# Optimization experiments

Measured on AMD Instinct MI355X. Metric: run time of the kernel, lower is better.

## Reference

```python
import jax, jax.numpy as jnp
import numpy as np

N = 4096        # nodes == batch_size (GFN operates on dense N x N adjacency)
E = 65536       # edges per view (avg degree 16)
IN = 512        # per-view input feature dim
HV = [128, 64]  # per-view GCN dims
HM = [64, 64]   # fused-graph GCN dims
VIEWS = 3


def setup_inputs() -> dict:
    key = jax.random.key(0)
    ks = iter(jax.random.split(key, 64))

    def xavier(shape):
        lim = float(np.sqrt(6.0 / (shape[0] + shape[1])))
        return jax.random.uniform(next(ks), shape, minval=-lim, maxval=lim, dtype=jnp.float32)

    inp = {}
    for v in range(VIEWS):
        inp[f"x{v}"] = jax.random.normal(next(ks), (N, IN), dtype=jnp.float32)
        inp[f"src{v}"] = jax.random.randint(next(ks), (E,), 0, N, dtype=jnp.int32)
        inp[f"dst{v}"] = jax.random.randint(next(ks), (E,), 0, N, dtype=jnp.int32)
        inp[f"Wv{v}0"] = xavier((IN, HV[0]))
        inp[f"bv{v}0"] = jnp.zeros((HV[0],), jnp.float32)
        inp[f"Wv{v}1"] = xavier((HV[0], HV[1]))
        inp[f"bv{v}1"] = jnp.zeros((HV[1],), jnp.float32)
        inp[f"Wf{v}"] = xavier((HV[1], HV[1]))  # FeatureFusion weight
    # GFN: Linear(N -> N/2) -> ReLU -> Linear(N/2 -> N)
    inp["Wg1"] = xavier((N, N // 2)); inp["bg1"] = jnp.zeros((N // 2,), jnp.float32)
    inp["Wg2"] = xavier((N // 2, N)); inp["bg2"] = jnp.zeros((N,), jnp.float32)
    # fused-graph GCN layers
    inp["Wm0"] = xavier((HV[1], HM[0])); inp["bm0"] = jnp.zeros((HM[0],), jnp.float32)
    inp["Wm1"] = xavier((HM[0], HM[1])); inp["bm1"] = jnp.zeros((HM[1],), jnp.float32)
    return inp


def _deg_norms(src, dst):
    # DGL GraphConv norm='both': scale by out-deg(src)^-1/2 and in-deg(dst)^-1/2, degrees clamped to >=1
    ones = jnp.ones(src.shape[0], jnp.float32)
    dout = jnp.maximum(jax.ops.segment_sum(ones, src, num_segments=N), 1.0)
    din = jnp.maximum(jax.ops.segment_sum(ones, dst, num_segments=N), 1.0)
    return dout ** -0.5, din ** -0.5


def _gconv(x, W, b, src, dst, do_isqrt, di_isqrt, act):
    h = (x * do_isqrt[:, None]) @ W            # [N, out] (W commutes with row scaling)
    agg = jax.ops.segment_sum(h[src], dst, num_segments=N)
    h = agg * di_isqrt[:, None] + b
    return act(h)


def reference(x0, x1, x2, src0, dst0, src1, dst1, src2, dst2,
              Wv00, bv00, Wv01, bv01, Wv10, bv10, Wv11, bv11, Wv20, bv20, Wv21, bv21,
              Wf0, Wf1, Wf2, Wg1, bg1, Wg2, bg2, Wm0, bm0, Wm1, bm1):
    ident = lambda t: t
    xs = [x0, x1, x2]
    edges = [(src0, dst0), (src1, dst1), (src2, dst2)]
    Wv = [(Wv00, bv00, Wv01, bv01), (Wv10, bv10, Wv11, bv11), (Wv20, bv20, Wv21, bv21)]
    Wf = [Wf0, Wf1, Wf2]

    # per-view GCN stacks (relu on first layer, identity on last)
    feats = []
    for v in range(VIEWS):
        src, dst = edges[v]
        do_i, di_i = _deg_norms(src, dst)
        W0, b0, W1, b1 = Wv[v]
        f = _gconv(xs[v], W0, b0, src, dst, do_i, di_i, jax.nn.relu)
        f = _gconv(f, W1, b1, src, dst, do_i, di_i, ident)
        feats.append(f)

    # FeatureFusion (dropout omitted for determinism): sum(f @ Wf), softmax over features, relu
    z = feats[0] @ Wf[0] + feats[1] @ Wf[1] + feats[2] @ Wf[2]
    z = jax.nn.relu(jax.nn.softmax(z, axis=1))

    # consensus graph: sum of per-view dense adjacencies -> GFN -> clamp -> round(+0.1)
    adj = jnp.zeros((N, N), jnp.float32)
    for src, dst in edges:
        adj = adj + jnp.zeros((N, N), jnp.float32).at[src, dst].set(1.0)
    fused = jax.nn.relu(adj @ Wg1 + bg1) @ Wg2 + bg2
    fused = jnp.round(jnp.clip(fused, 0.0, 1.0) + 0.1)
    adj_r = fused

    # rebuild binary graph (went through numpy in original -> stop_gradient), symmetrize, add self-loops
    sym = jax.lax.stop_gradient(fused)
    sym = sym + sym.T
    A = jnp.maximum((sym > 0).astype(jnp.float32), jnp.eye(N, dtype=jnp.float32))
    deg = A.sum(axis=1)
    dn = deg ** -0.5

    # fused-graph GCN layers (dense normalized SpMM form since A is already dense)
    h = z
    h = jax.nn.relu(((A @ (h * dn[:, None])) * dn[:, None]) @ Wm0 + bm0)
    h = ((A @ (h * dn[:, None])) * dn[:, None]) @ Wm1 + bm1

    # InnerProductDecoder with identity activation; all `views` entries of adj_rec are identical
    adj_rec = h @ h.T
    return (adj_r, adj_rec, h)
```

## Files before the change

### kernel.cpp

```cpp
#include <hip/hip_runtime.h>
#include <math.h>

#define NNODES 4096
#define NEDGES 65536

typedef short bf16x8 __attribute__((ext_vector_type(8)));
typedef short short4v __attribute__((ext_vector_type(4)));
typedef float f32x4 __attribute__((ext_vector_type(4)));

struct Ptr3  { const float* p[3]; };
struct Ptr3i { const int*   p[3]; };
struct Ptr3h { const short* p[3]; };

__device__ __forceinline__ short f2bf(float f) {
    unsigned u = __builtin_bit_cast(unsigned, f);
    unsigned r = (u + 0x7FFFu + ((u >> 16) & 1u)) >> 16;
    return (short)r;
}
__device__ __forceinline__ float bf2f(short s) {
    return __builtin_bit_cast(float, ((unsigned)(unsigned short)s) << 16);
}

__device__ __forceinline__ void gload_lds16(const void* g, void* l) {
    __builtin_amdgcn_global_load_lds(
        (const __attribute__((address_space(1))) unsigned*)g,
        (__attribute__((address_space(3))) unsigned*)l, 16, 0, 0);
}

template<int ACT>
__global__ __launch_bounds__(512, 1)
void gm_k(const short* __restrict__ A, const short* __restrict__ Bt,
          const float* __restrict__ bias, void* __restrict__ Cout, void* __restrict__ Cout1,
          unsigned char* __restrict__ Pout, int M, int Nn, int K, int lda, int ldb)
{
    constexpr int SLOT = 32768;
    __shared__ short lds[2 * SLOT];
    const int tid = threadIdx.x;
    const int lane = tid & 63;
    const int wave = tid >> 6;
    const int wm = wave >> 2, wn = wave & 3;
    const int z = blockIdx.z;
    A  += (size_t)z * K;
    Bt += (size_t)z * K;
    void* Cw = (ACT == 3 && z == 1) ? Cout1 : Cout;
    const int gx = gridDim.x, nwg = gx * gridDim.y;
    int w = blockIdx.y * gx + blockIdx.x;
    const int q8 = nwg >> 3;
    w = (w & 7) * q8 + (w >> 3);
    const int bm0 = (w / gx) * 256, bn0 = (w % gx) * 256;
    const int NT = K >> 6;

    auto stageH = [&](int t, int part) {
        if (t >= NT) return;
        const int k0 = t << 6;
        char* base = (char*)(lds + (t & 1) * SLOT);
        const int isB = (part < 2);
        const int h = part & 1;
#pragma unroll
        for (int r = 0; r < 2; ++r) {
            int o = r * 8192 + tid * 16;
            int row = o >> 7;
            int grow = h * 128 + row;
            int scol = (((o >> 4) & 7) ^ (grow & 7)) << 3;
            const short* gsrc = isB ? (Bt + (size_t)(bn0 + grow) * ldb + k0 + scol)
                                    : (A  + (size_t)(bm0 + grow) * lda + k0 + scol);
            gload_lds16(gsrc, base + (isB ? 32768 : 0) + h * 16384 + r * 8192 + wave * 1024);
        }
    };

    f32x4 acc[8][4] = {};
    bf16x8 aF[4][2];
    bf16x8 bF[4][2];

#define PH(QM, QN, TCUR, T1, P1, T2, P2, VM)                                          \
    {                                                                                 \
        const short* As_ = lds + ((TCUR) & 1) * SLOT;                                 \
        const short* Bs_ = As_ + 16384;                                               \
        if constexpr ((QN) == 0) {                                                    \
            _Pragma("unroll") for (int kk = 0; kk < 2; ++kk) {                        \
                const int h_ = kk * 4 + (lane >> 4);                                  \
                _Pragma("unroll") for (int i = 0; i < 4; ++i) {                       \
                    int r_ = wm * 128 + (QM) * 64 + i * 16 + (lane & 15);             \
                    aF[i][kk] = *(const bf16x8*)(As_ + r_ * 64 + ((h_ ^ (r_ & 7)) << 3)); \
                }                                                                     \
            }                                                                         \
        }                                                                             \
        if constexpr ((QM) == 0) {                                                    \
            _Pragma("unroll") for (int kk = 0; kk < 2; ++kk) {                        \
                const int h_ = kk * 4 + (lane >> 4);                                  \
                _Pragma("unroll") for (int j = 0; j < 2; ++j) {                       \
                    int r_ = wn * 64 + ((QN) * 2 + j) * 16 + (lane & 15);             \
                    bF[(QN) * 2 + j][kk] = *(const bf16x8*)(Bs_ + r_ * 64 + ((h_ ^ (r_ & 7)) << 3)); \
                }                                                                     \
            }                                                                         \
        }                                                                             \
        if ((P1) >= 0) stageH(T1, P1);                                                \
        if ((P2) >= 0) stageH(T2, P2);                                                \
        if constexpr ((QM) == 0 && (QN) == 0) {                                       \
            asm volatile("s_waitcnt lgkmcnt(8)" ::: "memory");                        \
        }                                                                             \
        __builtin_amdgcn_s_barrier();                                                 \
        __builtin_amdgcn_s_setprio(1);                                                \
        _Pragma("unroll") for (int kk = 0; kk < 2; ++kk)                              \
            _Pragma("unroll") for (int i = 0; i < 4; ++i)                             \
                _Pragma("unroll") for (int j = 0; j < 2; ++j)                         \
                    acc[(QM) * 4 + i][(QN) * 2 + j] =                                 \
                        __builtin_amdgcn_mfma_f32_16x16x32_bf16(                      \
                            aF[i][kk], bF[(QN) * 2 + j][kk],                          \
                            acc[(QM) * 4 + i][(QN) * 2 + j], 0, 0, 0);                \
        __builtin_amdgcn_s_setprio(0);                                                \
        if ((VM) == 6)      { asm volatile("s_waitcnt vmcnt(6)" ::: "memory");        \
                              __builtin_amdgcn_sched_barrier(0); }                    \
        else if ((VM) == 0) { asm volatile("s_waitcnt vmcnt(0)" ::: "memory");        \
                              __builtin_amdgcn_sched_barrier(0); }                    \
        __builtin_amdgcn_s_barrier();                                                 \
    }

    stageH(0, 0); stageH(0, 1); stageH(0, 2); stageH(0, 3);
    if (NT > 1) { stageH(1, 0); stageH(1, 1); stageH(1, 2); }
    if (NT > 1) { asm volatile("s_waitcnt vmcnt(6)" ::: "memory"); }
    else        { asm volatile("s_waitcnt vmcnt(0)" ::: "memory"); }
    __builtin_amdgcn_sched_barrier(0);
    __builtin_amdgcn_s_barrier();

    for (int it = 0; it < NT / 2; ++it) {
        const int t0 = 2 * it, t1 = t0 + 1, t2 = t0 + 2, t3 = t0 + 3;
        const int vm4 = (t2 < NT) ? 6 : 0;
        const int vm8 = (t3 < NT) ? 6 : 0;
        PH(0, 0, t0, t1, 3,  0, -1, -1)
        PH(0, 1, t0,  0, -1, 0, -1, -1)
        PH(1, 0, t0, t2, 0, t2,  1, -1)
        PH(1, 1, t0, t2, 2,  0, -1, vm4)
        PH(0, 0, t1, t2, 3,  0, -1, -1)
        PH(0, 1, t1,  0, -1, 0, -1, -1)
        PH(1, 0, t1, t3, 0, t3,  1, -1)
        PH(1, 1, t1, t3, 2,  0, -1, vm8)
    }
    if (NT & 1) {
        const int tl = NT - 1;
        PH(0, 0, tl, 0, -1, 0, -1, -1)
        PH(0, 1, tl, 0, -1, 0, -1, -1)
        PH(1, 0, tl, 0, -1, 0, -1, -1)
        PH(1, 1, tl, 0, -1, 0, -1, -1)
    }
#undef PH

    const int cr = (lane >> 4) * 4;
    const int cc = lane & 15;
#pragma unroll
    for (int im = 0; im < 8; ++im) {
#pragma unroll
        for (int jn = 0; jn < 4; ++jn) {
            int col = bn0 + wn * 64 + jn * 16 + cc;
            float bv = bias ? bias[col] : 0.f;
#pragma unroll
            for (int q2 = 0; q2 < 4; ++q2) {
                int row = bm0 + wm * 128 + (im >> 2) * 64 + (im & 3) * 16 + cr + q2;
                float v = acc[im][jn][q2] + bv;
                if constexpr (ACT == 2) {
                    v = rintf(fminf(fmaxf(v, 0.f), 1.f) + 0.1f);
                    ((float*)Cw)[(size_t)row * Nn + col] = v;
                    Pout[(size_t)row * Nn + col] = (unsigned char)(v > 0.5f);
                } else if constexpr (ACT == 3) {
                    ((short*)Cw)[(size_t)row * Nn + col] = f2bf(v);
                } else {
                    ((float*)Cw)[(size_t)row * Nn + col] = v;
                }
            }
        }
    }
}

__global__ void reduce_h1_k(const short* __restrict__ p0, const short* __restrict__ p1,
                            const float* __restrict__ bias, short* __restrict__ H1b)
{
    int i = (blockIdx.x * 256 + threadIdx.x) * 8;
    bf16x8 a = *(const bf16x8*)(p0 + i);
    bf16x8 b = *(const bf16x8*)(p1 + i);
    int col = i & 2047;
    bf16x8 o;
#pragma unroll
    for (int j = 0; j < 8; ++j) {
        float v = bf2f(a[j]) + bf2f(b[j]) + bias[col + j];
        o[j] = f2bf(fmaxf(v, 0.f));
    }
    *(bf16x8*)(H1b + i) = o;
}

__global__ void edge_k(Ptr3i src, Ptr3i dst, unsigned* __restrict__ mask, int* __restrict__ degs)
{
    int e = blockIdx.x * 256 + threadIdx.x;
    int z = blockIdx.y;
    if (e < NEDGES) {
        int s = src.p[z][e], d = dst.p[z][e];
        unsigned c = (unsigned)s * (unsigned)NNODES + (unsigned)d;
        atomicOr(&mask[c >> 2], 1u << ((c & 3u) * 8u + (unsigned)z));
        atomicAdd(&degs[2 * z * NNODES + s], 1);
        atomicAdd(&degs[(2 * z + 1) * NNODES + d], 1);
    }
}

__global__ __launch_bounds__(1024)
void scan_k(const int* __restrict__ degs, float* __restrict__ isq,
            int* __restrict__ rowptr, int* __restrict__ cursor)
{
    const int z = blockIdx.x;
    const int* dout = degs + 2 * z * NNODES;
    const int* din = degs + (2 * z + 1) * NNODES;
    const int t = threadIdx.x;
    for (int i = t; i < NNODES; i += 1024) {
        isq[2 * z * NNODES + i]       = 1.0f / sqrtf(fmaxf((float)dout[i], 1.0f));
        isq[(2 * z + 1) * NNODES + i] = 1.0f / sqrtf(fmaxf((float)din[i], 1.0f));
    }
    __shared__ int sm[1024];
    int v0 = din[t * 4], v1 = din[t * 4 + 1], v2 = din[t * 4 + 2], v3 = din[t * 4 + 3];
    int c1 = v0 + v1, c2 = c1 + v2, s = c2 + v3;
    sm[t] = s;
    __syncthreads();
    for (int off = 1; off < 1024; off <<= 1) {
        int add = (t >= off) ? sm[t - off] : 0;
        __syncthreads();
        sm[t] += add;
        __syncthreads();
    }
    int base = sm[t] - s;
    int* rp = rowptr + z * NNODES;
    int* cu = cursor + z * NNODES;
    rp[t * 4] = base;          cu[t * 4] = base;
    rp[t * 4 + 1] = base + v0; cu[t * 4 + 1] = base + v0;
    rp[t * 4 + 2] = base + c1; cu[t * 4 + 2] = base + c1;
    rp[t * 4 + 3] = base + c2; cu[t * 4 + 3] = base + c2;
}

__global__ void fill_k(Ptr3i src, Ptr3i dst, int* __restrict__ cursor, int* __restrict__ eidx)
{
    int e = blockIdx.x * 256 + threadIdx.x;
    int z = blockIdx.y;
    if (e < NEDGES) {
        int d = dst.p[z][e];
        int pos = atomicAdd(&cursor[z * NNODES + d], 1);
        eidx[(size_t)z * NEDGES + pos] = src.p[z][e];
    }
}

__device__ __forceinline__ void wsplit_body(const float* __restrict__ W, int K, int Nn,
                                            short* __restrict__ out, int idx)
{
    int k = idx / Nn, n = idx % Nn;
    float w = W[(size_t)k * Nn + n];
    short hi = f2bf(w);
    short lo = f2bf(w - bf2f(hi));
    short* row = out + (size_t)n * 3 * K;
    row[k] = hi; row[K + k] = lo; row[2 * K + k] = hi;
}

__global__ void prep_pv_k(Ptr3 xv, Ptr3 w0, Ptr3 w1, Ptr3 wf, const float* __restrict__ isq,
                          short* __restrict__ xe, short* __restrict__ Wv0T,
                          short* __restrict__ Wv1T, short* __restrict__ WfT)
{
    const int b = blockIdx.x;
    const int tid = threadIdx.x;
    if (b < 24576) {
        int z = b / 8192;
        int t = (b % 8192) * 256 + tid;
        int n = t >> 9, k = t & 511;
        float a = xv.p[z][(size_t)n * 512 + k] * isq[2 * z * NNODES + n];
        short hi = f2bf(a);
        short lo = f2bf(a - bf2f(hi));
        short* row = xe + (size_t)z * NNODES * 1536 + (size_t)n * 1536;
        row[k] = hi; row[512 + k] = hi; row[1024 + k] = lo;
    } else if (b < 24576 + 768) {
        int i = b - 24576;
        int z = i / 256;
        wsplit_body(w0.p[z], 512, 128, Wv0T + (size_t)z * 128 * 1536, (i % 256) * 256 + tid);
    } else if (b < 24576 + 768 + 96) {
        int i = b - 24576 - 768;
        int z = i / 32;
        wsplit_body(w1.p[z], 128, 64, Wv1T + (size_t)z * 64 * 384, (i % 32) * 256 + tid);
    } else {
        int i = b - 24576 - 768 - 96;
        int z = i / 16;
        wsplit_body(wf.p[z], 64, 64, WfT + (size_t)z * 64 * 192, (i % 16) * 256 + tid);
    }
}

__global__ __launch_bounds__(256)
void prep_gfn_k(const unsigned* __restrict__ mask, short* __restrict__ AdjB,
                const float* __restrict__ Wg1, short* __restrict__ Wg1T,
                const float* __restrict__ Wg2, short* __restrict__ Wg2T)
{
    __shared__ float tlds[64][65];
    const int b = blockIdx.x;
    const int tid = threadIdx.x;
    if (b < 16384) {
        int t = b * 256 + tid;
        unsigned w = mask[t];
        short4v o;
        o.x = f2bf((float)__popc(w & 0x7u));
        o.y = f2bf((float)__popc(w & 0x700u));
        o.z = f2bf((float)__popc(w & 0x70000u));
        o.w = f2bf((float)__popc(w & 0x7000000u));
        *(short4v*)(AdjB + (size_t)t * 4) = o;
        return;
    }
    const float* src; short* dstT; int R, C, bx, by;
    if (b < 16384 + 2048) {
        int i = b - 16384; bx = i % 32; by = i / 32;
        src = Wg1; dstT = Wg1T; R = 4096; C = 2048;
    } else {
        int i = b - 16384 - 2048; bx = i % 64; by = i / 64;
        src = Wg2; dstT = Wg2T; R = 2048; C = 4096;
    }
    const int br = by * 64, bc = bx * 64;
    for (int idx = tid; idx < 64 * 64; idx += 256) {
        int r = idx >> 6, c = idx & 63;
        tlds[r][c] = src[(size_t)(br + r) * C + bc + c];
    }
    __syncthreads();
    for (int idx = tid; idx < 64 * 64; idx += 256) {
        int c = idx >> 6, r = idx & 63;
        dstT[(size_t)(bc + c) * R + br + r] = f2bf(tlds[r][c]);
    }
}

__global__ __launch_bounds__(256)
void mfma_gemm_b_k(const short* __restrict__ Aall, Ptr3h Btv, float* __restrict__ Call,
                   int M, int Nn, int K)
{
    __shared__ short As[64 * 64];
    __shared__ short Bs[64 * 64];
    const int z = blockIdx.z;
    const short* A = Aall + (size_t)z * M * K;
    const short* Bt = Btv.p[z];
    float* C = Call + (size_t)z * M * Nn;
    const int tid = threadIdx.x;
    const int lane = tid & 63, wave = tid >> 6;
    const int bm0 = blockIdx.y * 64, bn0 = blockIdx.x * 64;
    const int wr = (wave >> 1) * 32, wc = (wave & 1) * 32;

    f32x4 acc[2][2] = {};

    for (int k0 = 0; k0 < K; k0 += 64) {
        for (int c = wave; c < 8; c += 4) {
            int o = c * 1024 + lane * 16;
            int row = o >> 7;
            int sl = (o >> 4) & 7;
            int ss = sl ^ (row & 7);
            gload_lds16(A + ((size_t)(bm0 + row) * K + k0 + ss * 8), As + c * 512);
            gload_lds16(Bt + ((size_t)(bn0 + row) * K + k0 + ss * 8), Bs + c * 512);
        }
        __syncthreads();
#pragma unroll
        for (int kk = 0; kk < 2; ++kk) {
            bf16x8 a[2], b[2];
            const int khalf = kk * 4 + (lane >> 4);
#pragma unroll
            for (int i = 0; i < 2; ++i) {
                int r = wr + i * 16 + (lane & 15);
                a[i] = *(const bf16x8*)(As + r * 64 + ((khalf ^ (r & 7)) << 3));
            }
#pragma unroll
            for (int j = 0; j < 2; ++j) {
                int r = wc + j * 16 + (lane & 15);
                b[j] = *(const bf16x8*)(Bs + r * 64 + ((khalf ^ (r & 7)) << 3));
            }
#pragma unroll
            for (int i = 0; i < 2; ++i)
#pragma unroll
                for (int j = 0; j < 2; ++j)
                    acc[i][j] = __builtin_amdgcn_mfma_f32_16x16x32_bf16(a[i], b[j], acc[i][j], 0, 0, 0);
        }
        __syncthreads();
    }

    const int cr = (lane >> 4) * 4;
    const int cc = lane & 15;
#pragma unroll
    for (int i = 0; i < 2; ++i)
#pragma unroll
        for (int j = 0; j < 2; ++j)
#pragma unroll
            for (int q = 0; q < 4; ++q) {
                int row = bm0 + wr + i * 16 + cr + q;
                int col = bn0 + wc + j * 16 + cc;
                C[(size_t)row * Nn + col] = acc[i][j][q];
            }
}

__global__ __launch_bounds__(256)
void spmm_mfma_k(const unsigned char* __restrict__ A8, const short* __restrict__ XsT,
                 float* __restrict__ part)
{
    __shared__ short As[64 * 64];
    __shared__ short Bs[128 * 64];
    const int tid = threadIdx.x;
    const int lane = tid & 63, wave = tid >> 6;
    const int kc = blockIdx.x, m0 = blockIdx.y * 64;
    const int wr = (wave >> 1) * 32, wc = (wave & 1) * 32;
    const int woff = wave * 512;

    f32x4 acc[2][2] = {};

    for (int k0 = kc * 512; k0 < kc * 512 + 512; k0 += 64) {
        {
            int row = tid >> 2, cb = (tid & 3) * 16;
            uint4 wv = *(const uint4*)(A8 + (size_t)(m0 + row) * 4096 + k0 + cb);
            unsigned wa[4] = {wv.x, wv.y, wv.z, wv.w};
            bf16x8 v0, v1;
#pragma unroll
            for (int bb = 0; bb < 8; ++bb)
                v0[bb] = ((wa[bb >> 2] >> ((bb & 3) * 8)) & 0xFFu) ? (short)0x3F80 : (short)0;
#pragma unroll
            for (int bb = 0; bb < 8; ++bb)
                v1[bb] = ((wa[2 + (bb >> 2)] >> ((bb & 3) * 8)) & 0xFFu) ? (short)0x3F80 : (short)0;
            int s0 = (tid & 3) * 2;
            *(bf16x8*)(As + row * 64 + ((s0 ^ (row & 7)) << 3)) = v0;
            *(bf16x8*)(As + row * 64 + (((s0 + 1) ^ (row & 7)) << 3)) = v1;
        }
#pragma unroll
        for (int r = 0; r < 4; ++r) {
            int o = r * 4096 + tid * 16;
            int row = o >> 7;
            int sl = (o >> 4) & 7;
            gload_lds16(XsT + ((size_t)row * 4096 + k0 + ((sl ^ (row & 7)) << 3)),
                        Bs + r * 2048 + woff);
        }
        __syncthreads();
#pragma unroll
        for (int kk = 0; kk < 2; ++kk) {
            const int h = kk * 4 + (lane >> 4);
            bf16x8 a[2], bh[2], bl[2];
#pragma unroll
            for (int i = 0; i < 2; ++i) {
                int r = wr + i * 16 + (lane & 15);
                a[i] = *(const bf16x8*)(As + r * 64 + ((h ^ (r & 7)) << 3));
            }
#pragma unroll
            for (int j = 0; j < 2; ++j) {
                int r = wc + j * 16 + (lane & 15);
                bh[j] = *(const bf16x8*)(Bs + r * 64 + ((h ^ (r & 7)) << 3));
                int r2 = r + 64;
                bl[j] = *(const bf16x8*)(Bs + r2 * 64 + ((h ^ (r2 & 7)) << 3));
            }
#pragma unroll
            for (int i = 0; i < 2; ++i)
#pragma unroll
                for (int j = 0; j < 2; ++j) {
                    acc[i][j] = __builtin_amdgcn_mfma_f32_16x16x32_bf16(a[i], bh[j], acc[i][j], 0, 0, 0);
                    acc[i][j] = __builtin_amdgcn_mfma_f32_16x16x32_bf16(a[i], bl[j], acc[i][j], 0, 0, 0);
                }
        }
        __syncthreads();
    }

    const int cr = (lane >> 4) * 4;
    const int cc = lane & 15;
#pragma unroll
    for (int i = 0; i < 2; ++i)
#pragma unroll
        for (int j = 0; j < 2; ++j)
#pragma unroll
            for (int q = 0; q < 4; ++q)
                part[((size_t)kc * NNODES + m0 + wr + i * 16 + cr + q) * 64 + wc + j * 16 + cc]
                    = acc[i][j][q];
}

__global__ void xsT_k(const float* __restrict__ X, const int* __restrict__ degA,
                      short* __restrict__ XsT)
{
    const int n = blockIdx.y;
    const int k = blockIdx.x * 256 + threadIdx.x;
    float v = X[(size_t)k * 64 + n] * (1.0f / sqrtf((float)degA[k]));
    short hi = f2bf(v);
    short lo = f2bf(v - bf2f(hi));
    XsT[(size_t)n * 4096 + k] = hi;
    XsT[(size_t)(64 + n) * 4096 + k] = lo;
}

template<int RELU>
__global__ __launch_bounds__(256)
void redgemm_k(const float* __restrict__ part, const int* __restrict__ degA,
               const float* __restrict__ Wm, const float* __restrict__ bias,
               float* __restrict__ out, short* __restrict__ Ae, short* __restrict__ Be,
               short* __restrict__ XsT)
{
    __shared__ float Ws[64 * 64];
    const int tid = threadIdx.x;
    for (int i = tid; i < 4096; i += 256) Ws[i] = Wm[i];
    __syncthreads();
    const int lane = tid & 63, wave = tid >> 6;
    const float bv = bias[lane];
    for (int rr = 0; rr < 4; ++rr) {
        int row = blockIdx.x * 16 + wave * 4 + rr;
        float s = 0.f;
#pragma unroll
        for (int p = 0; p < 8; ++p) s += part[((size_t)p * NNODES + row) * 64 + lane];
        const float dn = 1.0f / sqrtf((float)degA[row]);
        s *= dn;
        float acc = bv;
#pragma unroll
        for (int k = 0; k < 64; ++k)
            acc = fmaf(__shfl(s, k), Ws[k * 64 + lane], acc);
        if (RELU) acc = fmaxf(acc, 0.f);
        out[(size_t)row * 64 + lane] = acc;
        if (Ae) {
            short hi = f2bf(acc);
            short lo = f2bf(acc - bf2f(hi));
            size_t ro = (size_t)row * 192;
            Ae[ro + lane] = hi; Ae[ro + 64 + lane] = hi; Ae[ro + 128 + lane] = lo;
            Be[ro + lane] = hi; Be[ro + 64 + lane] = lo; Be[ro + 128 + lane] = hi;
        }
        if (XsT) {
            float vv = acc * dn;
            short hi = f2bf(vv);
            short lo = f2bf(vv - bf2f(hi));
            XsT[(size_t)lane * 4096 + row] = hi;
            XsT[(size_t)(64 + lane) * 4096 + row] = lo;
        }
    }
}

template<int F, int ACT, int MODE>
__global__ void gather_k(const float* __restrict__ Hpre, const int* __restrict__ eidx,
                         const int* __restrict__ rowptr, const int* __restrict__ degs,
                         const float* __restrict__ isq, Ptr3 bias, short* __restrict__ Sout)
{
    const int z = blockIdx.y;
    const int tid = threadIdx.x;
    const int node = blockIdx.x * (256 / F) + tid / F;
    const int f = tid % F;
    const float* H = Hpre + (size_t)z * NNODES * F;
    const int base = rowptr[z * NNODES + node];
    const int cnt = degs[(2 * z + 1) * NNODES + node];
    const int* ei = eidx + (size_t)z * NEDGES + base;
    float s = 0.f;
    for (int i = 0; i < cnt; ++i) s += H[(size_t)ei[i] * F + f];
    float v = s * isq[(2 * z + 1) * NNODES + node] + bias.p[z][f];
    if (ACT) v = fmaxf(v, 0.f);
    if (MODE == 1) v *= isq[2 * z * NNODES + node];
    short hi = f2bf(v);
    short lo = f2bf(v - bf2f(hi));
    short* row = Sout + (size_t)z * NNODES * 3 * F + (size_t)node * 3 * F;
    row[f] = hi; row[F + f] = hi; row[2 * F + f] = lo;
}

__global__ void softsum_k(const float* __restrict__ zp, float* __restrict__ z)
{
    int row = blockIdx.x * 4 + (threadIdx.x >> 6);
    int f = threadIdx.x & 63;
    size_t i = (size_t)row * 64 + f;
    float v = zp[i] + zp[i + (size_t)NNODES * 64] + zp[i + (size_t)2 * NNODES * 64];
    float m = v;
#pragma unroll
    for (int off = 32; off >= 1; off >>= 1) m = fmaxf(m, __shfl_xor(m, off));
    float e = expf(v - m);
    float s = e;
#pragma unroll
    for (int off = 32; off >= 1; off >>= 1) s += __shfl_xor(s, off);
    z[i] = e / s;
}

__global__ __launch_bounds__(256)
void build_A2_k(const unsigned char* __restrict__ P, unsigned char* __restrict__ A8,
                int* __restrict__ degA)
{
    __shared__ unsigned Ts[64][20];
    const int bi = blockIdx.y * 64, bj = blockIdx.x * 64;
    const int tid = threadIdx.x;
    const int r = tid >> 2, seg = tid & 3;
    uint4 tv = *(const uint4*)(P + (size_t)(bj + r) * NNODES + bi + seg * 16);
    Ts[r][seg * 4 + 0] = tv.x; Ts[r][seg * 4 + 1] = tv.y;
    Ts[r][seg * 4 + 2] = tv.z; Ts[r][seg * 4 + 3] = tv.w;
    __syncthreads();
    uint4 dv = *(const uint4*)(P + (size_t)(bi + r) * NNODES + bj + seg * 16);
    unsigned dw[4] = {dv.x, dv.y, dv.z, dv.w};
    const unsigned char* Tb = (const unsigned char*)Ts;
    unsigned ow[4];
    int psum = 0;
#pragma unroll
    for (int w = 0; w < 4; ++w) {
        unsigned o = 0;
#pragma unroll
        for (int b = 0; b < 4; ++b) {
            int j = seg * 16 + w * 4 + b;
            unsigned a = (dw[w] >> (8 * b)) & 1u;
            unsigned tr = Tb[j * 80 + r] & 1u;
            unsigned on = a | tr | (unsigned)((bi + r) == (bj + j));
            o |= on << (8 * b);
            psum += (int)on;
        }
        ow[w] = o;
    }
    uint4 o4; o4.x = ow[0]; o4.y = ow[1]; o4.z = ow[2]; o4.w = ow[3];
    *(uint4*)(A8 + (size_t)(bi + r) * NNODES + bj + seg * 16) = o4;
    psum += __shfl_xor(psum, 1);
    psum += __shfl_xor(psum, 2);
    if (seg == 0) atomicAdd(&degA[bi + r], psum);
}

extern "C" void kernel_launch(void* const* d_in, const int* in_sizes, int n_in,
                              void* d_out, int out_size, void* d_ws, size_t ws_size,
                              hipStream_t stream)
{
    const int N = NNODES, E = NEDGES;
    const size_t MB = 1024 * 1024;

    const float* x[3]; const int* src[3]; const int* dst[3];
    const float *Wv0[3], *bv0[3], *Wv1[3], *bv1[3], *Wf[3];
    for (int v = 0; v < 3; ++v) {
        const int b = v * 8;
        x[v]   = (const float*)d_in[b + 0];
        src[v] = (const int*)  d_in[b + 1];
        dst[v] = (const int*)  d_in[b + 2];
        Wv0[v] = (const float*)d_in[b + 3];
        bv0[v] = (const float*)d_in[b + 4];
        Wv1[v] = (const float*)d_in[b + 5];
        bv1[v] = (const float*)d_in[b + 6];
        Wf[v]  = (const float*)d_in[b + 7];
    }
    const float* Wg1 = (const float*)d_in[24];
    const float* bg1 = (const float*)d_in[25];
    const float* Wg2 = (const float*)d_in[26];
    const float* bg2 = (const float*)d_in[27];
    const float* Wm0 = (const float*)d_in[28];
    const float* bm0 = (const float*)d_in[29];
    const float* Wm1 = (const float*)d_in[30];
    const float* bm1 = (const float*)d_in[31];

    float* out_adjr = (float*)d_out;
    float* out_rec  = out_adjr + (size_t)N * N;
    float* out_h    = out_rec + (size_t)N * N;

    char* oa = (char*)out_adjr;
    short* AdjB = (short*)oa;
    float* hv1  = (float*)(oa + 32 * MB);
    short* Ae2  = (short*)(oa + 38 * MB);
    short* Ae3  = (short*)(oa + 47 * MB);
    float* hv2  = (float*)(oa + 52 * MB);
    float* zp   = (float*)(oa + 56 * MB);
    short* partg0 = (short*)(oa + 32 * MB);
    short* partg1 = (short*)(oa + 48 * MB);

    char* orc = (char*)out_rec;
    short* xe   = (short*)orc;
    short* H1b  = (short*)orc;
    unsigned char* P = (unsigned char*)(orc + 16 * MB);
    float* part = (float*)(orc + 48 * MB);

    char* p = (char*)d_ws;
    unsigned* mask = (unsigned*)p;
    short* AeF = (short*)p;
    short* BeF = AeF + (size_t)N * 192;
    p += (size_t)N * N;
    int* degs = (int*)p;     p += (size_t)6 * N * 4;
    int* degA = (int*)p;     p += (size_t)N * 4;
    float* isq = (float*)p;  p += (size_t)6 * N * 4;
    int* rowptr = (int*)p;   p += (size_t)3 * N * 4;
    int* cursor = (int*)p;   p += (size_t)3 * N * 4;
    int* eidx = (int*)p;     p += (size_t)3 * E * 4;
    float* zbuf = (float*)p; p += (size_t)N * 64 * 4;
    float* h1m = (float*)p;  p += (size_t)N * 64 * 4;
    short* XsT = (short*)p;  p += (size_t)128 * N * 2;
    short* Wv0T = (short*)p; p += (size_t)3 * 128 * 1536 * 2;
    short* Wv1T = (short*)p; p += (size_t)3 * 64 * 384 * 2;
    short* WfT  = (short*)p; p += (size_t)3 * 64 * 192 * 2;
    unsigned char* A8 = (unsigned char*)d_ws + 64 * MB;
    short* Wg1T = (short*)((char*)d_ws + 96 * MB);
    short* Wg2T = (short*)((char*)d_ws + 112 * MB);

    Ptr3i srcP, dstP;
    for (int v = 0; v < 3; ++v) { srcP.p[v] = src[v]; dstP.p[v] = dst[v]; }

    hipMemsetAsync(mask, 0, (size_t)N * N + (size_t)7 * N * 4, stream);

    edge_k<<<dim3((E + 255) / 256, 3), 256, 0, stream>>>(srcP, dstP, mask, degs);
    scan_k<<<3, 1024, 0, stream>>>(degs, isq, rowptr, cursor);
    fill_k<<<dim3((E + 255) / 256, 3), 256, 0, stream>>>(srcP, dstP, cursor, eidx);

    prep_gfn_k<<<16384 + 2048 + 2048, 256, 0, stream>>>(mask, AdjB, Wg1, Wg1T, Wg2, Wg2T);

    Ptr3 xP, w0P, w1P, wfP;
    for (int v = 0; v < 3; ++v) { xP.p[v] = x[v]; w0P.p[v] = Wv0[v]; w1P.p[v] = Wv1[v]; wfP.p[v] = Wf[v]; }
    prep_pv_k<<<24576 + 768 + 96 + 48, 256, 0, stream>>>(xP, w0P, w1P, wfP, isq,
                                                          xe, Wv0T, Wv1T, WfT);

    Ptr3h BtP; Ptr3 biasP;
    for (int v = 0; v < 3; ++v) BtP.p[v] = Wv0T + (size_t)v * 128 * 1536;
    mfma_gemm_b_k<<<dim3(2, N / 64, 3), 256, 0, stream>>>(xe, BtP, hv1, N, 128, 1536);
    for (int v = 0; v < 3; ++v) biasP.p[v] = bv0[v];
    gather_k<128, 1, 1><<<dim3(N / 2, 3), 256, 0, stream>>>(hv1, eidx, rowptr, degs, isq, biasP, Ae2);
    for (int v = 0; v < 3; ++v) BtP.p[v] = Wv1T + (size_t)v * 64 * 384;
    mfma_gemm_b_k<<<dim3(1, N / 64, 3), 256, 0, stream>>>(Ae2, BtP, hv2, N, 64, 384);
    for (int v = 0; v < 3; ++v) biasP.p[v] = bv1[v];
    gather_k<64, 0, 2><<<dim3(N / 4, 3), 256, 0, stream>>>(hv2, eidx, rowptr, degs, isq, biasP, Ae3);
    for (int v = 0; v < 3; ++v) BtP.p[v] = WfT + (size_t)v * 64 * 192;
    mfma_gemm_b_k<<<dim3(1, N / 64, 3), 256, 0, stream>>>(Ae3, BtP, zp, N, 64, 192);
    softsum_k<<<N / 4, 256, 0, stream>>>(zp, zbuf);

    gm_k<3><<<dim3(2048 / 256, 4096 / 256, 2), 512, 0, stream>>>(
        AdjB, Wg1T, nullptr, partg0, partg1, nullptr, 4096, 2048, 2048, 4096, 4096);
    reduce_h1_k<<<4096 * 2048 / 8 / 256, 256, 0, stream>>>(partg0, partg1, bg1, H1b);

    gm_k<2><<<dim3(4096 / 256, 4096 / 256, 1), 512, 0, stream>>>(
        H1b, Wg2T, bg2, out_adjr, nullptr, P, 4096, 4096, 2048, 2048, 2048);

    build_A2_k<<<dim3(N / 64, N / 64), 256, 0, stream>>>(P, A8, degA);

    xsT_k<<<dim3(16, 64), 256, 0, stream>>>(zbuf, degA, XsT);
    spmm_mfma_k<<<dim3(8, N / 64), 256, 0, stream>>>(A8, XsT, part);
    redgemm_k<1><<<256, 256, 0, stream>>>(part, degA, Wm0, bm0, h1m, nullptr, nullptr, XsT);
    spmm_mfma_k<<<dim3(8, N / 64), 256, 0, stream>>>(A8, XsT, part);
    redgemm_k<0><<<256, 256, 0, stream>>>(part, degA, Wm1, bm1, out_h, AeF, BeF, nullptr);

    gm_k<0><<<dim3(4096 / 256, 4096 / 256, 1), 512, 0, stream>>>(
        AeF, BeF, nullptr, out_rec, nullptr, nullptr, 4096, 4096, 192, 192, 192);
}
```

Before: 427.7 us.

## Merge prep kernels and fuse X scaling/bf16 split into SpMM B-tile load

New measurement: 467.1 us. +9.2%, slower.

```diff
diff --git a/kernel.cpp b/kernel.cpp
--- a/kernel.cpp
+++ b/kernel.cpp
@@ -254,40 +254,13 @@
     row[k] = hi; row[K + k] = lo; row[2 * K + k] = hi;
 }
 
-__global__ void prep_pv_k(Ptr3 xv, Ptr3 w0, Ptr3 w1, Ptr3 wf, const float* __restrict__ isq,
-                          short* __restrict__ xe, short* __restrict__ Wv0T,
-                          short* __restrict__ Wv1T, short* __restrict__ WfT)
-{
-    const int b = blockIdx.x;
-    const int tid = threadIdx.x;
-    if (b < 24576) {
-        int z = b / 8192;
-        int t = (b % 8192) * 256 + tid;
-        int n = t >> 9, k = t & 511;
-        float a = xv.p[z][(size_t)n * 512 + k] * isq[2 * z * NNODES + n];
-        short hi = f2bf(a);
-        short lo = f2bf(a - bf2f(hi));
-        short* row = xe + (size_t)z * NNODES * 1536 + (size_t)n * 1536;
-        row[k] = hi; row[512 + k] = hi; row[1024 + k] = lo;
-    } else if (b < 24576 + 768) {
-        int i = b - 24576;
-        int z = i / 256;
-        wsplit_body(w0.p[z], 512, 128, Wv0T + (size_t)z * 128 * 1536, (i % 256) * 256 + tid);
-    } else if (b < 24576 + 768 + 96) {
-        int i = b - 24576 - 768;
-        int z = i / 32;
-        wsplit_body(w1.p[z], 128, 64, Wv1T + (size_t)z * 64 * 384, (i % 32) * 256 + tid);
-    } else {
-        int i = b - 24576 - 768 - 96;
-        int z = i / 16;
-        wsplit_body(wf.p[z], 64, 64, WfT + (size_t)z * 64 * 192, (i % 16) * 256 + tid);
-    }
-}
-
 __global__ __launch_bounds__(256)
-void prep_gfn_k(const unsigned* __restrict__ mask, short* __restrict__ AdjB,
+void prep_all_k(const unsigned* __restrict__ mask, short* __restrict__ AdjB,
                 const float* __restrict__ Wg1, short* __restrict__ Wg1T,
-                const float* __restrict__ Wg2, short* __restrict__ Wg2T)
+                const float* __restrict__ Wg2, short* __restrict__ Wg2T,
+                Ptr3 xv, Ptr3 w0, Ptr3 w1, Ptr3 wf, const float* __restrict__ isq,
+                short* __restrict__ xe, short* __restrict__ Wv0T,
+                short* __restrict__ Wv1T, short* __restrict__ WfT)
 {
     __shared__ float tlds[64][65];
     const int b = blockIdx.x;
@@ -303,23 +276,49 @@
         *(short4v*)(AdjB + (size_t)t * 4) = o;
         return;
     }
-    const float* src; short* dstT; int R, C, bx, by;
-    if (b < 16384 + 2048) {
-        int i = b - 16384; bx = i % 32; by = i / 32;
-        src = Wg1; dstT = Wg1T; R = 4096; C = 2048;
+    if (b < 20480) {
+        const float* src; short* dstT; int R, C, bx, by;
+        if (b < 16384 + 2048) {
+            int i = b - 16384; bx = i % 32; by = i / 32;
+            src = Wg1; dstT = Wg1T; R = 4096; C = 2048;
+        } else {
+            int i = b - 16384 - 2048; bx = i % 64; by = i / 64;
+            src = Wg2; dstT = Wg2T; R = 2048; C = 4096;
+        }
+        const int br = by * 64, bc = bx * 64;
+        for (int idx = tid; idx < 64 * 64; idx += 256) {
+            int r = idx >> 6, c = idx & 63;
+            tlds[r][c] = src[(size_t)(br + r) * C + bc + c];
+        }
+        __syncthreads();
+        for (int idx = tid; idx < 64 * 64; idx += 256) {
+            int c = idx >> 6, r = idx & 63;
+            dstT[(size_t)(bc + c) * R + br + r] = f2bf(tlds[r][c]);
+        }
+        return;
+    }
+    if (b < 20480 + 24576) {
+        int i = b - 20480;
+        int z = i / 8192;
+        int t = (i % 8192) * 256 + tid;
+        int n = t >> 9, k = t & 511;
+        float a = xv.p[z][(size_t)n * 512 + k] * isq[2 * z * NNODES + n];
+        short hi = f2bf(a);
+        short lo = f2bf(a - bf2f(hi));
+        short* row = xe + (size_t)z * NNODES * 1536 + (size_t)n * 1536;
+        row[k] = hi; row[512 + k] = hi; row[1024 + k] = lo;
+    } else if (b < 20480 + 24576 + 768) {
+        int i = b - 20480 - 24576;
+        int z = i / 256;
+        wsplit_body(w0.p[z], 512, 128, Wv0T + (size_t)z * 128 * 1536, (i % 256) * 256 + tid);
+    } else if (b < 20480 + 24576 + 768 + 96) {
+        int i = b - 20480 - 24576 - 768;
+        int z = i / 32;
+        wsplit_body(w1.p[z], 128, 64, Wv1T + (size_t)z * 64 * 384, (i % 32) * 256 + tid);
     } else {
-        int i = b - 16384 - 2048; bx = i % 64; by = i / 64;
-        src = Wg2; dstT = Wg2T; R = 2048; C = 4096;
-    }
-    const int br = by * 64, bc = bx * 64;
-    for (int idx = tid; idx < 64 * 64; idx += 256) {
-        int r = idx >> 6, c = idx & 63;
-        tlds[r][c] = src[(size_t)(br + r) * C + bc + c];
-    }
-    __syncthreads();
-    for (int idx = tid; idx < 64 * 64; idx += 256) {
-        int c = idx >> 6, r = idx & 63;
-        dstT[(size_t)(bc + c) * R + br + r] = f2bf(tlds[r][c]);
+        int i = b - 20480 - 24576 - 768 - 96;
+        int z = i / 16;
+        wsplit_body(wf.p[z], 64, 64, WfT + (size_t)z * 64 * 192, (i % 16) * 256 + tid);
     }
 }
 
@@ -388,8 +387,8 @@
 }
 
 __global__ __launch_bounds__(256)
-void spmm_mfma_k(const unsigned char* __restrict__ A8, const short* __restrict__ XsT,
-                 float* __restrict__ part)
+void spmm_mfma_k(const unsigned char* __restrict__ A8, const float* __restrict__ X,
+                 const int* __restrict__ degA, float* __restrict__ part)
 {
     __shared__ short As[64 * 64];
     __shared__ short Bs[128 * 64];
@@ -397,7 +396,6 @@
     const int lane = tid & 63, wave = tid >> 6;
     const int kc = blockIdx.x, m0 = blockIdx.y * 64;
     const int wr = (wave >> 1) * 32, wc = (wave & 1) * 32;
-    const int woff = wave * 512;
 
     f32x4 acc[2][2] = {};
 
@@ -417,13 +415,25 @@
             *(bf16x8*)(As + row * 64 + ((s0 ^ (row & 7)) << 3)) = v0;
             *(bf16x8*)(As + row * 64 + (((s0 + 1) ^ (row & 7)) << 3)) = v1;
         }
-#pragma unroll
-        for (int r = 0; r < 4; ++r) {
-            int o = r * 4096 + tid * 16;
-            int row = o >> 7;
-            int sl = (o >> 4) & 7;
-            gload_lds16(XsT + ((size_t)row * 4096 + k0 + ((sl ^ (row & 7)) << 3)),
-                        Bs + r * 2048 + woff);
+        {
+            const int n = tid & 63;
+            const int kkb = (tid >> 6) * 16;
+#pragma unroll
+            for (int s = 0; s < 2; ++s) {
+                bf16x8 vh, vl;
+#pragma unroll
+                for (int j = 0; j < 8; ++j) {
+                    int k = k0 + kkb + s * 8 + j;
+                    float v = X[(size_t)k * 64 + n] * (1.0f / sqrtf((float)degA[k]));
+                    short hi = f2bf(v);
+                    vh[j] = hi;
+                    vl[j] = f2bf(v - bf2f(hi));
+                }
+                int slot = (kkb >> 3) + s;
+                *(bf16x8*)(Bs + n * 64 + ((slot ^ (n & 7)) << 3)) = vh;
+                int r2 = 64 + n;
+                *(bf16x8*)(Bs + r2 * 64 + ((slot ^ (r2 & 7)) << 3)) = vl;
+            }
         }
         __syncthreads();
 #pragma unroll
@@ -465,24 +475,11 @@
                     = acc[i][j][q];
 }
 
-__global__ void xsT_k(const float* __restrict__ X, const int* __restrict__ degA,
-                      short* __restrict__ XsT)
-{
-    const int n = blockIdx.y;
-    const int k = blockIdx.x * 256 + threadIdx.x;
-    float v = X[(size_t)k * 64 + n] * (1.0f / sqrtf((float)degA[k]));
-    short hi = f2bf(v);
-    short lo = f2bf(v - bf2f(hi));
-    XsT[(size_t)n * 4096 + k] = hi;
-    XsT[(size_t)(64 + n) * 4096 + k] = lo;
-}
-
 template<int RELU>
 __global__ __launch_bounds__(256)
 void redgemm_k(const float* __restrict__ part, const int* __restrict__ degA,
                const float* __restrict__ Wm, const float* __restrict__ bias,
-               float* __restrict__ out, short* __restrict__ Ae, short* __restrict__ Be,
-               short* __restrict__ XsT)
+               float* __restrict__ out, short* __restrict__ Ae, short* __restrict__ Be)
 {
     __shared__ float Ws[64 * 64];
     const int tid = threadIdx.x;
@@ -509,13 +506,6 @@
             size_t ro = (size_t)row * 192;
             Ae[ro + lane] = hi; Ae[ro + 64 + lane] = hi; Ae[ro + 128 + lane] = lo;
             Be[ro + lane] = hi; Be[ro + 64 + lane] = lo; Be[ro + 128 + lane] = hi;
-        }
-        if (XsT) {
-            float vv = acc * dn;
-            short hi = f2bf(vv);
-            short lo = f2bf(vv - bf2f(hi));
-            XsT[(size_t)lane * 4096 + row] = hi;
-            XsT[(size_t)(64 + lane) * 4096 + row] = lo;
         }
     }
 }
@@ -660,7 +650,6 @@
     int* eidx = (int*)p;     p += (size_t)3 * E * 4;
     float* zbuf = (float*)p; p += (size_t)N * 64 * 4;
     float* h1m = (float*)p;  p += (size_t)N * 64 * 4;
-    short* XsT = (short*)p;  p += (size_t)128 * N * 2;
     short* Wv0T = (short*)p; p += (size_t)3 * 128 * 1536 * 2;
     short* Wv1T = (short*)p; p += (size_t)3 * 64 * 384 * 2;
     short* WfT  = (short*)p; p += (size_t)3 * 64 * 192 * 2;
@@ -675,14 +664,13 @@
 
     edge_k<<<dim3((E + 255) / 256, 3), 256, 0, stream>>>(srcP, dstP, mask, degs);
     scan_k<<<3, 1024, 0, stream>>>(degs, isq, rowptr, cursor);
-    fill_k<<<dim3((E + 255) / 256, 3), 256, 0, stream>>>(srcP, dstP, cursor, eidx);
-
-    prep_gfn_k<<<16384 + 2048 + 2048, 256, 0, stream>>>(mask, AdjB, Wg1, Wg1T, Wg2, Wg2T);
 
     Ptr3 xP, w0P, w1P, wfP;
     for (int v = 0; v < 3; ++v) { xP.p[v] = x[v]; w0P.p[v] = Wv0[v]; w1P.p[v] = Wv1[v]; wfP.p[v] = Wf[v]; }
-    prep_pv_k<<<24576 + 768 + 96 + 48, 256, 0, stream>>>(xP, w0P, w1P, wfP, isq,
-                                                          xe, Wv0T, Wv1T, WfT);
+    prep_all_k<<<20480 + 24576 + 768 + 96 + 48, 256, 0, stream>>>(
+        mask, AdjB, Wg1, Wg1T, Wg2, Wg2T, xP, w0P, w1P, wfP, isq, xe, Wv0T, Wv1T, WfT);
+
+    fill_k<<<dim3((E + 255) / 256, 3), 256, 0, stream>>>(srcP, dstP, cursor, eidx);
 
     Ptr3h BtP; Ptr3 biasP;
     for (int v = 0; v < 3; ++v) BtP.p[v] = Wv0T + (size_t)v * 128 * 1536;
@@ -706,11 +694,10 @@
 
     build_A2_k<<<dim3(N / 64, N / 64), 256, 0, stream>>>(P, A8, degA);
 
-    xsT_k<<<dim3(16, 64), 256, 0, stream>>>(zbuf, degA, XsT);
-    spmm_mfma_k<<<dim3(8, N / 64), 256, 0, stream>>>(A8, XsT, part);
-    redgemm_k<1><<<256, 256, 0, stream>>>(part, degA, Wm0, bm0, h1m, nullptr, nullptr, XsT);
-    spmm_mfma_k<<<dim3(8, N / 64), 256, 0, stream>>>(A8, XsT, part);
-    redgemm_k<0><<<256, 256, 0, stream>>>(part, degA, Wm1, bm1, out_h, AeF, BeF, nullptr);
+    spmm_mfma_k<<<dim3(8, N / 64), 256, 0, stream>>>(A8, zbuf, degA, part);
+    redgemm_k<1><<<256, 256, 0, stream>>>(part, degA, Wm0, bm0, h1m, nullptr, nullptr);
+    spmm_mfma_k<<<dim3(8, N / 64), 256, 0, stream>>>(A8, h1m, degA, part);
+    redgemm_k<0><<<256, 256, 0, stream>>>(part, degA, Wm1, bm1, out_h, AeF, BeF);
 
     gm_k<0><<<dim3(4096 / 256, 4096 / 256, 1), 512, 0, stream>>>(
         AeF, BeF, nullptr, out_rec, nullptr, nullptr, 4096, 4096, 192, 192, 192);
```
